# Optimization experiments

Measured on AMD Instinct MI355X. Metric: run time of the kernel, lower is better.

Reference implementation:

```python
import jax, jax.numpy as jnp
import numpy as np

B, IN, H = 8192, 1024, 1024


def setup_inputs() -> dict:
    key = jax.random.key(0)
    kx, kh, kc, kwx, kwh = jax.random.split(key, 5)
    return {
        "x": jax.random.normal(kx, (B, IN), dtype=jnp.float32),
        "h": jax.random.normal(kh, (B, H), dtype=jnp.float32),
        "c": jax.random.normal(kc, (B, H), dtype=jnp.float32),
        # 8 Dense layers fused: gate order [i, f, g, o] along last axis
        "Wx": jax.random.normal(kwx, (IN, 4 * H), dtype=jnp.float32) * 0.02,
        "Wh": jax.random.normal(kwh, (H, 4 * H), dtype=jnp.float32) * 0.02,
        "bx": jnp.zeros((4 * H,), dtype=jnp.float32),
        "bh": jnp.zeros((4 * H,), dtype=jnp.float32),
    }


def reference(x, h, c, Wx, Wh, bx, bh):
    # Fused equivalent of the 8 separate Dense layers:
    #   gate_k = x @ Wx[:, k] + bx[k] + h @ Wh[:, k] + bh[k]
    gates = x @ Wx + h @ Wh + (bx + bh)  # [B, 4H]
    i, f, g, o = jnp.split(gates, 4, axis=-1)
    i = jax.nn.sigmoid(i)
    f = jax.nn.sigmoid(f)
    g = jnp.tanh(g)
    o = jax.nn.sigmoid(o)
    c_new = f * c + i * g
    h_new = o * jnp.tanh(c_new)
    # Original returns (out_gate, hidden_state, cell_state)
    return (o, h_new, c_new)
```

## Files before the change

### kernel.cpp

```cpp
#include <hip/hip_runtime.h>
#include <hip/hip_bf16.h>

typedef __attribute__((ext_vector_type(8))) short bf16x8;
typedef __attribute__((ext_vector_type(4))) float f32x4;
typedef __attribute__((ext_vector_type(8))) unsigned short u16x8;

#define B_DIM 8192
#define H_DIM 1024
#define K_DIM 2048
#define N_DIM 4096
#define BH (B_DIM * H_DIM)
#define NT 32

__device__ __forceinline__ unsigned short f2bf(float f) {
    union { float f; unsigned u; } v; v.f = f;
    unsigned r = v.u + 0x7FFFu + ((v.u >> 16) & 1u);
    return (unsigned short)(r >> 16);
}

__device__ __forceinline__ void gload16(const void* g, void* l) {
    __builtin_amdgcn_global_load_lds(
        (const __attribute__((address_space(1))) void*)g,
        (__attribute__((address_space(3))) void*)l, 16, 0, 0);
}

__global__ void prep(const float* __restrict__ x, const float* __restrict__ h,
                     const float* __restrict__ Wx, const float* __restrict__ Wh,
                     unsigned short* __restrict__ Abf, unsigned short* __restrict__ Bperm) {
    __shared__ float tile[64][65];
    const int t = threadIdx.x;
    if (blockIdx.x < 8192) {
        int gid = blockIdx.x * 256 + t;
        size_t e = (size_t)gid * 8;
        int m   = gid >> 8;
        int col = (gid & 255) * 8;
        int p   = col >> 10;
        int k   = col & 1023;
        const float* src = (p ? h : x) + (size_t)m * 1024 + k;
        float4 v0 = *(const float4*)src;
        float4 v1 = *(const float4*)(src + 4);
        u16x8 o = { f2bf(v0.x), f2bf(v0.y), f2bf(v0.z), f2bf(v0.w),
                    f2bf(v1.x), f2bf(v1.y), f2bf(v1.z), f2bf(v1.w) };
        *(u16x8*)(Abf + e) = o;
        return;
    }
    const int bz = blockIdx.x - 8192;
    const int k0 = (bz & 31) * 64;
    const int n0 = (bz >> 5) * 64;
#pragma unroll
    for (int it = 0; it < 4; ++it) {
        int lin = it * 256 + t;
        int kl  = lin >> 4;
        int n4  = lin & 15;
        int k   = k0 + kl;
        const float* src = (k < 1024) ? (Wx + (size_t)k * 4096 + n0 + n4 * 4)
                                      : (Wh + (size_t)(k - 1024) * 4096 + n0 + n4 * 4);
        float4 v = *(const float4*)src;
        tile[kl][n4 * 4 + 0] = v.x;
        tile[kl][n4 * 4 + 1] = v.y;
        tile[kl][n4 * 4 + 2] = v.z;
        tile[kl][n4 * 4 + 3] = v.w;
    }
    __syncthreads();
#pragma unroll
    for (int it = 0; it < 2; ++it) {
        int lin = it * 256 + t;
        int nl  = lin >> 3;
        int ch  = lin & 7;
        int n    = n0 + nl;
        int gate = n >> 10;
        int j    = n & 1023;
        int jb   = j >> 5;
        int jj   = j & 31;
        int R    = jb * 128 + (jj >> 4) * 64 + gate * 16 + (jj & 15);
        u16x8 o;
#pragma unroll
        for (int q = 0; q < 8; ++q) o[q] = f2bf(tile[ch * 8 + q][nl]);
        *(u16x8*)(Bperm + (size_t)R * 2048 + k0 + ch * 8) = o;
    }
}

#define VMW(N) asm volatile("s_waitcnt vmcnt(" #N ")" ::: "memory")
#define BAR() __builtin_amdgcn_s_barrier()

#define LD_A(BUF, TMB) do { \
  _Pragma("unroll") \
  for (int _tm = 0; _tm < 4; ++_tm) \
    _Pragma("unroll") \
    for (int _ks = 0; _ks < 2; ++_ks) \
      af[(TMB) + _tm][_ks] = *(const bf16x8*)(lsA + (BUF) * 16384 + \
          (wm * 128 + ((TMB) + _tm) * 16 + fRow) * 64 + ((_ks * 4 + q4) ^ rx) * 8); \
} while (0)

#define LD_B(BUF, TNB) do { \
  _Pragma("unroll") \
  for (int _tn = 0; _tn < 2; ++_tn) \
    _Pragma("unroll") \
    for (int _ks = 0; _ks < 2; ++_ks) \
      bfr[_tn][_ks] = *(const bf16x8*)(lsB + (BUF) * 16384 + \
          (wn * 64 + ((TNB) + _tn) * 16 + fRow) * 64 + ((_ks * 4 + q4) ^ rx) * 8); \
} while (0)

#define STAGE_A(BUF, H, T) do { \
  gload16(Abf + (size_t)(m0 + (H) * 128 + sRow) * K_DIM + (T) * 64 + sChunk, \
          lsA + (BUF) * 16384 + (H) * 8192 + wave * 512); \
  gload16(Abf + (size_t)(m0 + (H) * 128 + 64 + sRow) * K_DIM + (T) * 64 + sChunk, \
          lsA + (BUF) * 16384 + (H) * 8192 + 4096 + wave * 512); \
} while (0)

#define STAGE_B(BUF, H, T) do { \
  gload16(Bperm + (size_t)(r0 + (H) * 128 + sRow) * K_DIM + (T) * 64 + sChunk, \
          lsB + (BUF) * 16384 + (H) * 8192 + wave * 512); \
  gload16(Bperm + (size_t)(r0 + (H) * 128 + 64 + sRow) * K_DIM + (T) * 64 + sChunk, \
          lsB + (BUF) * 16384 + (H) * 8192 + 4096 + wave * 512); \
} while (0)

#define MFMA_QUAD(TMB, TNB) do { \
  __builtin_amdgcn_s_setprio(1); \
  _Pragma("unroll") \
  for (int _ks = 0; _ks < 2; ++_ks) \
    _Pragma("unroll") \
    for (int _tm = 0; _tm < 4; ++_tm) \
      _Pragma("unroll") \
      for (int _tn = 0; _tn < 2; ++_tn) \
        acc[(TMB) + _tm][(TNB) + _tn] = __builtin_amdgcn_mfma_f32_16x16x32_bf16( \
            af[(TMB) + _tm][_ks], bfr[_tn][_ks], acc[(TMB) + _tm][(TNB) + _tn], 0, 0, 0); \
  __builtin_amdgcn_s_setprio(0); \
} while (0)

__global__ __launch_bounds__(512, 2) void lstm_fused(
    const unsigned short* __restrict__ Abf,
    const unsigned short* __restrict__ Bperm,
    const float* __restrict__ bx, const float* __restrict__ bh,
    const float* __restrict__ cin, float* __restrict__ out) {
    __shared__ unsigned short lsA[2 * 256 * 64];
    __shared__ unsigned short lsB[2 * 256 * 64];

    const int tid  = threadIdx.x;
    const int wave = tid >> 6;
    const int lane = tid & 63;
    const int wm   = wave >> 2;
    const int wn   = wave & 3;

    const int bid = blockIdx.x;
    const int swz = (bid & 7) * 64 + (bid >> 3);
    const int bm  = swz & 31;
    const int bn  = swz >> 5;
    const int m0  = bm * 256;
    const int r0  = bn * 256;

    const int sRow   = tid >> 3;
    const int sChunk = ((tid & 7) ^ ((tid >> 3) & 7)) * 8;

    const int fRow = lane & 15;
    const int q4   = lane >> 4;
    const int rx   = fRow & 7;

    f32x4 acc[8][4];
#pragma unroll
    for (int i = 0; i < 8; ++i)
#pragma unroll
        for (int j = 0; j < 4; ++j) acc[i][j] = (f32x4){0.f, 0.f, 0.f, 0.f};

    bf16x8 af[8][2];
    bf16x8 bfr[2][2];

    STAGE_A(0, 0, 0); STAGE_A(0, 1, 0); STAGE_B(0, 0, 0); STAGE_B(0, 1, 0);
    STAGE_A(1, 0, 1); STAGE_A(1, 1, 1);
    VMW(4);
    BAR();

    for (int i = 0; i < 15; ++i) {
        const int t = 2 * i;
        LD_A(0, 0); LD_B(0, 0);
        STAGE_B(1, 0, t + 1);
        BAR();
        MFMA_QUAD(0, 0);
        BAR();
        LD_A(0, 4);
        STAGE_B(1, 1, t + 1);
        BAR();
        MFMA_QUAD(4, 0);
        BAR();
        LD_B(0, 2);
        STAGE_A(0, 0, t + 2);
        BAR();
        MFMA_QUAD(4, 2);
        BAR();
        STAGE_A(0, 1, t + 2);
        BAR();
        MFMA_QUAD(0, 2);
        VMW(4);
        BAR();
        LD_A(1, 0); LD_B(1, 0);
        STAGE_B(0, 0, t + 2);
        BAR();
        MFMA_QUAD(0, 0);
        BAR();
        LD_A(1, 4);
        STAGE_B(0, 1, t + 2);
        BAR();
        MFMA_QUAD(4, 0);
        BAR();
        LD_B(1, 2);
        STAGE_A(1, 0, t + 3);
        BAR();
        MFMA_QUAD(4, 2);
        BAR();
        STAGE_A(1, 1, t + 3);
        BAR();
        MFMA_QUAD(0, 2);
        VMW(4);
        BAR();
    }

    STAGE_B(1, 0, 31); STAGE_B(1, 1, 31);
    LD_A(0, 0); LD_B(0, 0); MFMA_QUAD(0, 0);
    LD_A(0, 4);             MFMA_QUAD(4, 0);
    LD_B(0, 2);             MFMA_QUAD(4, 2); MFMA_QUAD(0, 2);
    VMW(0);
    BAR();
    LD_A(1, 0); LD_B(1, 0); MFMA_QUAD(0, 0);
    LD_A(1, 4);             MFMA_QUAD(4, 0);
    LD_B(1, 2);             MFMA_QUAD(4, 2); MFMA_QUAD(0, 2);

    const int j = bn * 64 + (wn >> 1) * 32 + (wn & 1) * 16 + fRow;
    const float b_i = bx[j] + bh[j];
    const float b_f = bx[1024 + j] + bh[1024 + j];
    const float b_g = bx[2048 + j] + bh[2048 + j];
    const float b_o = bx[3072 + j] + bh[3072 + j];
#pragma unroll
    for (int tm = 0; tm < 8; ++tm) {
#pragma unroll
        for (int r = 0; r < 4; ++r) {
            const int row = m0 + wm * 128 + tm * 16 + q4 * 4 + r;
            float vi = acc[tm][0][r] + b_i;
            float vf = acc[tm][1][r] + b_f;
            float vg = acc[tm][2][r] + b_g;
            float vo = acc[tm][3][r] + b_o;
            float ig = 1.f / (1.f + __expf(-vi));
            float fg = 1.f / (1.f + __expf(-vf));
            float e2g = __expf(2.f * fminf(fmaxf(vg, -15.f), 15.f));
            float gg = (e2g - 1.f) / (e2g + 1.f);
            float og = 1.f / (1.f + __expf(-vo));
            float cn = fg * cin[(size_t)row * 1024 + j] + ig * gg;
            float e2c = __expf(2.f * fminf(fmaxf(cn, -15.f), 15.f));
            float hn = og * ((e2c - 1.f) / (e2c + 1.f));
            out[(size_t)row * 1024 + j] = og;
            out[(size_t)BH + (size_t)row * 1024 + j] = hn;
            out[(size_t)2 * BH + (size_t)row * 1024 + j] = cn;
        }
    }
}

extern "C" void kernel_launch(void* const* d_in, const int* in_sizes, int n_in,
                              void* d_out, int out_size, void* d_ws, size_t ws_size,
                              hipStream_t stream) {
    const float* x  = (const float*)d_in[0];
    const float* h  = (const float*)d_in[1];
    const float* c  = (const float*)d_in[2];
    const float* Wx = (const float*)d_in[3];
    const float* Wh = (const float*)d_in[4];
    const float* bx = (const float*)d_in[5];
    const float* bh = (const float*)d_in[6];
    float* out = (float*)d_out;

    unsigned short* Abf   = (unsigned short*)d_ws;
    unsigned short* Bperm = (unsigned short*)((char*)d_ws + (size_t)B_DIM * K_DIM * 2);

    hipLaunchKernelGGL(prep, dim3(8192 + 2048), dim3(256), 0, stream, x, h, Wx, Wh, Abf, Bperm);
    hipLaunchKernelGGL(lstm_fused, dim3(512), dim3(512), 0, stream,
                       Abf, Bperm, bx, bh, c, out);
}
```

Before: 353.7 us.

## Split prep kernel, add explicit LDS waits, use nontemporal output stores

```diff
diff --git a/kernel.cpp b/kernel.cpp
--- a/kernel.cpp
+++ b/kernel.cpp
@@ -24,13 +24,12 @@
         (__attribute__((address_space(3))) void*)l, 16, 0, 0);
 }
 
-__global__ void prep(const float* __restrict__ x, const float* __restrict__ h,
-                     const float* __restrict__ Wx, const float* __restrict__ Wh,
-                     unsigned short* __restrict__ Abf, unsigned short* __restrict__ Bperm) {
-    __shared__ float tile[64][65];
-    const int t = threadIdx.x;
-    if (blockIdx.x < 8192) {
-        int gid = blockIdx.x * 256 + t;
+__global__ void prep_pack(const float* __restrict__ x, const float* __restrict__ h,
+                          unsigned short* __restrict__ Abf) {
+    const int gid0 = blockIdx.x * 256 + threadIdx.x;
+#pragma unroll
+    for (int it = 0; it < 4; ++it) {
+        int gid = gid0 + it * (2048 * 256);
         size_t e = (size_t)gid * 8;
         int m   = gid >> 8;
         int col = (gid & 255) * 8;
@@ -42,9 +41,14 @@
         u16x8 o = { f2bf(v0.x), f2bf(v0.y), f2bf(v0.z), f2bf(v0.w),
                     f2bf(v1.x), f2bf(v1.y), f2bf(v1.z), f2bf(v1.w) };
         *(u16x8*)(Abf + e) = o;
-        return;
-    }
-    const int bz = blockIdx.x - 8192;
+    }
+}
+
+__global__ void prep_w(const float* __restrict__ Wx, const float* __restrict__ Wh,
+                       unsigned short* __restrict__ Bperm) {
+    __shared__ float tile[64][65];
+    const int t  = threadIdx.x;
+    const int bz = blockIdx.x;
     const int k0 = (bz & 31) * 64;
     const int n0 = (bz >> 5) * 64;
 #pragma unroll
@@ -80,8 +84,9 @@
     }
 }
 
-#define VMW(N) asm volatile("s_waitcnt vmcnt(" #N ")" ::: "memory")
-#define BAR() __builtin_amdgcn_s_barrier()
+#define VMW(N)  asm volatile("s_waitcnt vmcnt(" #N ")" ::: "memory")
+#define LGKM0() asm volatile("s_waitcnt lgkmcnt(0)" ::: "memory")
+#define BAR()   __builtin_amdgcn_s_barrier()
 
 #define LD_A(BUF, TMB) do { \
   _Pragma("unroll") \
@@ -128,6 +133,15 @@
   __builtin_amdgcn_s_setprio(0); \
 } while (0)
 
+#define PHASE(LDS_OPS, STAGE_OP, TMB, TNB) do { \
+  LDS_OPS; \
+  STAGE_OP; \
+  BAR(); \
+  LGKM0(); \
+  MFMA_QUAD(TMB, TNB); \
+  BAR(); \
+} while (0)
+
 __global__ __launch_bounds__(512, 2) void lstm_fused(
     const unsigned short* __restrict__ Abf,
     const unsigned short* __restrict__ Bperm,
@@ -172,57 +186,35 @@
 
     for (int i = 0; i < 15; ++i) {
         const int t = 2 * i;
-        LD_A(0, 0); LD_B(0, 0);
-        STAGE_B(1, 0, t + 1);
-        BAR();
-        MFMA_QUAD(0, 0);
-        BAR();
-        LD_A(0, 4);
-        STAGE_B(1, 1, t + 1);
-        BAR();
-        MFMA_QUAD(4, 0);
-        BAR();
-        LD_B(0, 2);
-        STAGE_A(0, 0, t + 2);
-        BAR();
-        MFMA_QUAD(4, 2);
-        BAR();
+        PHASE(LD_A(0, 0); LD_B(0, 0), STAGE_B(1, 0, t + 1), 0, 0);
+        PHASE(LD_A(0, 4),             STAGE_B(1, 1, t + 1), 4, 0);
+        PHASE(LD_B(0, 2),             STAGE_A(0, 0, t + 2), 4, 2);
         STAGE_A(0, 1, t + 2);
         BAR();
+        LGKM0();
         MFMA_QUAD(0, 2);
         VMW(4);
         BAR();
-        LD_A(1, 0); LD_B(1, 0);
-        STAGE_B(0, 0, t + 2);
-        BAR();
-        MFMA_QUAD(0, 0);
-        BAR();
-        LD_A(1, 4);
-        STAGE_B(0, 1, t + 2);
-        BAR();
-        MFMA_QUAD(4, 0);
-        BAR();
-        LD_B(1, 2);
-        STAGE_A(1, 0, t + 3);
-        BAR();
-        MFMA_QUAD(4, 2);
-        BAR();
+        PHASE(LD_A(1, 0); LD_B(1, 0), STAGE_B(0, 0, t + 2), 0, 0);
+        PHASE(LD_A(1, 4),             STAGE_B(0, 1, t + 2), 4, 0);
+        PHASE(LD_B(1, 2),             STAGE_A(1, 0, t + 3), 4, 2);
         STAGE_A(1, 1, t + 3);
         BAR();
+        LGKM0();
         MFMA_QUAD(0, 2);
         VMW(4);
         BAR();
     }
 
     STAGE_B(1, 0, 31); STAGE_B(1, 1, 31);
-    LD_A(0, 0); LD_B(0, 0); MFMA_QUAD(0, 0);
-    LD_A(0, 4);             MFMA_QUAD(4, 0);
-    LD_B(0, 2);             MFMA_QUAD(4, 2); MFMA_QUAD(0, 2);
+    LD_A(0, 0); LD_B(0, 0); LGKM0(); MFMA_QUAD(0, 0);
+    LD_A(0, 4);             LGKM0(); MFMA_QUAD(4, 0);
+    LD_B(0, 2);             LGKM0(); MFMA_QUAD(4, 2); MFMA_QUAD(0, 2);
     VMW(0);
     BAR();
-    LD_A(1, 0); LD_B(1, 0); MFMA_QUAD(0, 0);
-    LD_A(1, 4);             MFMA_QUAD(4, 0);
-    LD_B(1, 2);             MFMA_QUAD(4, 2); MFMA_QUAD(0, 2);
+    LD_A(1, 0); LD_B(1, 0); LGKM0(); MFMA_QUAD(0, 0);
+    LD_A(1, 4);             LGKM0(); MFMA_QUAD(4, 0);
+    LD_B(1, 2);             LGKM0(); MFMA_QUAD(4, 2); MFMA_QUAD(0, 2);
 
     const int j = bn * 64 + (wn >> 1) * 32 + (wn & 1) * 16 + fRow;
     const float b_i = bx[j] + bh[j];
@@ -246,9 +238,9 @@
             float cn = fg * cin[(size_t)row * 1024 + j] + ig * gg;
             float e2c = __expf(2.f * fminf(fmaxf(cn, -15.f), 15.f));
             float hn = og * ((e2c - 1.f) / (e2c + 1.f));
-            out[(size_t)row * 1024 + j] = og;
-            out[(size_t)BH + (size_t)row * 1024 + j] = hn;
-            out[(size_t)2 * BH + (size_t)row * 1024 + j] = cn;
+            __builtin_nontemporal_store(og, out + (size_t)row * 1024 + j);
+            __builtin_nontemporal_store(hn, out + (size_t)BH + (size_t)row * 1024 + j);
+            __builtin_nontemporal_store(cn, out + (size_t)2 * BH + (size_t)row * 1024 + j);
         }
     }
 }
@@ -268,7 +260,8 @@
     unsigned short* Abf   = (unsigned short*)d_ws;
     unsigned short* Bperm = (unsigned short*)((char*)d_ws + (size_t)B_DIM * K_DIM * 2);
 
-    hipLaunchKernelGGL(prep, dim3(8192 + 2048), dim3(256), 0, stream, x, h, Wx, Wh, Abf, Bperm);
+    hipLaunchKernelGGL(prep_pack, dim3(2048), dim3(256), 0, stream, x, h, Abf);
+    hipLaunchKernelGGL(prep_w,    dim3(2048), dim3(256), 0, stream, Wx, Wh, Bperm);
     hipLaunchKernelGGL(lstm_fused, dim3(512), dim3(512), 0, stream,
                        Abf, Bperm, bx, bh, c, out);
 }
```

After: 358.9 us. Within noise of the previous version (+1.5%).
